# Kernel optimization log

Hardware: AMD Instinct MI355X
Metric: run time of the kernel (lower is better)

## Reference

```python
import jax, jax.numpy as jnp
import numpy as np

RATIO = 0.1

def setup_inputs() -> dict:
    key = jax.random.key(0)
    x = jax.random.normal(key, (8, 1024, 4096), dtype=jnp.float32)
    return {"x": x}

def reference(x):
    shape = x.shape
    xf = x.reshape(-1)                       # [N]
    k = int(RATIO * xf.shape[0])             # static k
    src, index = jax.lax.top_k(xf, k)         # values (not abs), matching torch.topk
    out = jnp.zeros_like(xf).at[index].set(src)
    return out.reshape(shape)
```

## Files before the change

### kernel.cpp

```cpp
#include <hip/hip_runtime.h>
#include <hip/hip_bf16.h>
#include <stdint.h>


#define STREAM_GRID 1024
#define STREAM_BLK  256
#define EQ_CAP      65536


__device__ __forceinline__ unsigned int f2u(float x) {
    unsigned int b = __float_as_uint(x);
    return (b & 0x80000000u) ? ~b : (b | 0x80000000u);
}

__global__ void init_kernel(unsigned int* sc, unsigned int k) {
    if (threadIdx.x == 0) {
        sc[0] = 0u; sc[1] = k; sc[2] = 0u; sc[3] = 0u; sc[4] = 0u;
    }
}

__global__ void __launch_bounds__(256)
hist_lds_kernel(const float* __restrict__ x, int n4, long long N,
                unsigned int* __restrict__ hist,
                const unsigned int* __restrict__ sc,
                int nbins, int shift, int match_shift)
{
    __shared__ unsigned int lh[4][2048];
    int tid = threadIdx.x;
    for (int i = tid; i < 4 * 2048; i += 256) ((unsigned int*)lh)[i] = 0u;
    const bool filt = (match_shift < 32);
    const int ms = filt ? match_shift : 0;
    unsigned int pref = 0u;
    if (filt) pref = sc[0] >> ms;
    __syncthreads();
    unsigned int* my = lh[tid >> 6];
    const float4* x4 = (const float4*)x;
    const unsigned int mask = (unsigned int)nbins - 1u;
    int stride = gridDim.x * blockDim.x;
    for (int i = blockIdx.x * blockDim.x + tid; i < n4; i += stride) {
        float4 v = x4[i];
        unsigned int u;
        u = f2u(v.x); if (!filt || ((u >> ms) == pref)) atomicAdd(&my[(u >> shift) & mask], 1u);
        u = f2u(v.y); if (!filt || ((u >> ms) == pref)) atomicAdd(&my[(u >> shift) & mask], 1u);
        u = f2u(v.z); if (!filt || ((u >> ms) == pref)) atomicAdd(&my[(u >> shift) & mask], 1u);
        u = f2u(v.w); if (!filt || ((u >> ms) == pref)) atomicAdd(&my[(u >> shift) & mask], 1u);
    }
    long long t0 = (long long)n4 * 4;
    if (blockIdx.x == 0 && tid < (int)(N - t0)) {
        unsigned int u = f2u(x[t0 + tid]);
        if (!filt || ((u >> ms) == pref)) atomicAdd(&my[(u >> shift) & mask], 1u);
    }
    __syncthreads();
    for (int i = tid; i < nbins; i += 256) {
        unsigned int s = lh[0][i] + lh[1][i] + lh[2][i] + lh[3][i];
        if (s) atomicAdd(&hist[i], s);
    }
}

__global__ void __launch_bounds__(256)
hist21_kernel(const float* __restrict__ x, int n4, long long N,
              unsigned int* __restrict__ hist2,
              const unsigned int* __restrict__ sc)
{
    unsigned int b1 = sc[0] >> 21;
    const float4* x4 = (const float4*)x;
    int stride = gridDim.x * blockDim.x;
    for (int i = blockIdx.x * blockDim.x + threadIdx.x; i < n4; i += stride) {
        float4 v = x4[i];
        unsigned int u;
        u = f2u(v.x); if ((u >> 21) == b1) atomicAdd(&hist2[u & 0x1FFFFFu], 1u);
        u = f2u(v.y); if ((u >> 21) == b1) atomicAdd(&hist2[u & 0x1FFFFFu], 1u);
        u = f2u(v.z); if ((u >> 21) == b1) atomicAdd(&hist2[u & 0x1FFFFFu], 1u);
        u = f2u(v.w); if ((u >> 21) == b1) atomicAdd(&hist2[u & 0x1FFFFFu], 1u);
    }
    long long t0 = (long long)n4 * 4;
    if (blockIdx.x == 0 && threadIdx.x < (int)(N - t0)) {
        unsigned int u = f2u(x[t0 + threadIdx.x]);
        if ((u >> 21) == b1) atomicAdd(&hist2[u & 0x1FFFFFu], 1u);
    }
}

__device__ __forceinline__ unsigned int block_exscan256(unsigned int v,
                                                        volatile unsigned int* lds,
                                                        int tid)
{
    lds[tid] = v;
    __syncthreads();
    for (int off = 1; off < 256; off <<= 1) {
        unsigned int t = (tid >= off) ? lds[tid - off] : 0u;
        __syncthreads();
        lds[tid] += t;
        __syncthreads();
    }
    unsigned int incl = lds[tid];
    return incl - v;
}

__global__ void __launch_bounds__(256)
scan_kernel(unsigned int* __restrict__ hist, int nbins, int shift, int is_final,
            unsigned int* __restrict__ sc)
{
    __shared__ unsigned int lds[256];
    int tid = threadIdx.x;
    int seg = nbins >> 8;
    unsigned int prefix = sc[0];
    unsigned int krem = sc[1];
    unsigned int loc[8];
    unsigned int partial = 0u;
    for (int i = 0; i < seg; ++i) {
        int p = tid * seg + i;
        unsigned int v = hist[nbins - 1 - p];
        loc[i] = v; partial += v;
    }
    unsigned int cum = block_exscan256(partial, lds, tid);
    for (int i = 0; i < seg; ++i) {
        int p = tid * seg + i;
        int bin = nbins - 1 - p;
        unsigned int c = loc[i];
        if (cum < krem && cum + c >= krem) {
            if (is_final) { sc[2] = prefix | ((unsigned int)bin << shift); sc[3] = krem - cum; }
            else          { sc[0] = prefix | ((unsigned int)bin << shift); sc[1] = krem - cum; }
        }
        cum += c;
    }
    for (int i = 0; i < seg; ++i) hist[nbins - 1 - (tid * seg + i)] = 0u;
}

__global__ void __launch_bounds__(256)
chunksum_kernel(const unsigned int* __restrict__ hist2, unsigned int* __restrict__ chunk_sums)
{
    __shared__ unsigned int p[256];
    int tid = threadIdx.x;
    int chunk = blockIdx.x;
    const unsigned int* base = hist2 + (size_t)chunk * 1024;
    unsigned int s = 0u;
    for (int i = tid; i < 1024; i += 256) s += base[i];
    p[tid] = s;
    __syncthreads();
    for (int off = 128; off; off >>= 1) {
        if (tid < off) p[tid] += p[tid + off];
        __syncthreads();
    }
    if (tid == 0) chunk_sums[chunk] = p[0];
}

__global__ void __launch_bounds__(256)
scanA_final_kernel(const unsigned int* __restrict__ hist2,
                   const unsigned int* __restrict__ chunk_sums,
                   unsigned int* __restrict__ sc)
{
    __shared__ unsigned int lds[256];
    __shared__ unsigned int s_c, s_krem2;
    int tid = threadIdx.x;
    unsigned int prefix = sc[0];
    unsigned int krem = sc[1];
    unsigned int loc[8];
    unsigned int partial = 0u;
    for (int i = 0; i < 8; ++i) {
        int p = tid * 8 + i;
        unsigned int v = chunk_sums[2047 - p];
        loc[i] = v; partial += v;
    }
    unsigned int cum = block_exscan256(partial, lds, tid);
    for (int i = 0; i < 8; ++i) {
        int p = tid * 8 + i;
        int chunk = 2047 - p;
        unsigned int c = loc[i];
        if (cum < krem && cum + c >= krem) { s_c = (unsigned int)chunk; s_krem2 = krem - cum; }
        cum += c;
    }
    __syncthreads();
    unsigned int c = s_c;
    unsigned int krem2 = s_krem2;
    unsigned int loc2[4];
    partial = 0u;
    for (int i = 0; i < 4; ++i) {
        int p = tid * 4 + i;
        unsigned int v = hist2[(size_t)c * 1024 + (1023 - p)];
        loc2[i] = v; partial += v;
    }
    __syncthreads();
    unsigned int cum2 = block_exscan256(partial, lds, tid);
    for (int i = 0; i < 4; ++i) {
        int p = tid * 4 + i;
        int bin = 1023 - p;
        unsigned int cc = loc2[i];
        if (cum2 < krem2 && cum2 + cc >= krem2) {
            sc[2] = prefix | (c * 1024u + (unsigned int)bin);
            sc[3] = krem2 - cum2;
        }
        cum2 += cc;
    }
}

__global__ void __launch_bounds__(256)
scatter_kernel(const float* __restrict__ x, int n4, long long N,
               float* __restrict__ out,
               unsigned int* __restrict__ sc,
               unsigned int* __restrict__ eq_list, int cap)
{
    unsigned int tu = sc[2];
    const float4* x4 = (const float4*)x;
    float4* o4 = (float4*)out;
    int stride = gridDim.x * blockDim.x;
    for (int i = blockIdx.x * blockDim.x + threadIdx.x; i < n4; i += stride) {
        float4 v = x4[i];
        unsigned int u0 = f2u(v.x), u1 = f2u(v.y), u2 = f2u(v.z), u3 = f2u(v.w);
        float4 o;
        o.x = (u0 > tu) ? v.x : 0.0f;
        o.y = (u1 > tu) ? v.y : 0.0f;
        o.z = (u2 > tu) ? v.z : 0.0f;
        o.w = (u3 > tu) ? v.w : 0.0f;
        if (u0 == tu || u1 == tu || u2 == tu || u3 == tu) {
            unsigned int b = (unsigned int)i * 4u;
            if (u0 == tu) { unsigned int p = atomicAdd(&sc[4], 1u); if (p < (unsigned int)cap) eq_list[p] = b + 0u; }
            if (u1 == tu) { unsigned int p = atomicAdd(&sc[4], 1u); if (p < (unsigned int)cap) eq_list[p] = b + 1u; }
            if (u2 == tu) { unsigned int p = atomicAdd(&sc[4], 1u); if (p < (unsigned int)cap) eq_list[p] = b + 2u; }
            if (u3 == tu) { unsigned int p = atomicAdd(&sc[4], 1u); if (p < (unsigned int)cap) eq_list[p] = b + 3u; }
        }
        o4[i] = o;
    }
    long long t0 = (long long)n4 * 4;
    if (blockIdx.x == 0 && threadIdx.x < (int)(N - t0)) {
        long long idx = t0 + threadIdx.x;
        float v = x[idx];
        unsigned int u = f2u(v);
        out[idx] = (u > tu) ? v : 0.0f;
        if (u == tu) { unsigned int p = atomicAdd(&sc[4], 1u); if (p < (unsigned int)cap) eq_list[p] = (unsigned int)idx; }
    }
}

__global__ void __launch_bounds__(256)
eqfix_kernel(float* __restrict__ out, const unsigned int* __restrict__ sc,
             const unsigned int* __restrict__ eq_list, int cap)
{
    unsigned int m = sc[4];
    if (m > (unsigned int)cap) m = (unsigned int)cap;
    unsigned int need = sc[3];
    unsigned int tu = sc[2];
    float f = __uint_as_float((tu & 0x80000000u) ? (tu & 0x7FFFFFFFu) : ~tu);
    for (unsigned int j = threadIdx.x; j < m; j += blockDim.x) {
        unsigned int idx = eq_list[j];
        unsigned int cnt = 0u;
        for (unsigned int l = 0; l < m; ++l) cnt += (eq_list[l] < idx) ? 1u : 0u;
        if (cnt < need) out[idx] = f;
    }
}

extern "C" void kernel_launch(void* const* d_in, const int* in_sizes, int n_in,
                              void* d_out, int out_size, void* d_ws, size_t ws_size,
                              hipStream_t stream) {
    const float* x = (const float*)d_in[0];
    float* out = (float*)d_out;
    long long N = (long long)in_sizes[0];
    int n4 = (int)(N >> 2);
    unsigned int k = (unsigned int)((double)N * 0.1);
    if (k == 0u) k = 1u;

    uint8_t* w = (uint8_t*)d_ws;
    unsigned int* sc         = (unsigned int*)(w);
    unsigned int* hist1      = (unsigned int*)(w + 256);
    unsigned int* chunk_sums = (unsigned int*)(w + 256 + 8192);
    unsigned int* eq_list    = (unsigned int*)(w + 256 + 16384);
    size_t baseB = 256 + 16384 + 262144;
    unsigned int* hist2      = (unsigned int*)(w + baseB);
    size_t needA = baseB + ((size_t)1 << 21) * sizeof(unsigned int);
    bool planA = (ws_size >= needA);

    int grid = STREAM_GRID;

    hipMemsetAsync(hist1, 0, 2048 * sizeof(unsigned int), stream);
    init_kernel<<<1, 64, 0, stream>>>(sc, k);

    if (planA) {
        hipMemsetAsync(hist2, 0, ((size_t)1 << 21) * sizeof(unsigned int), stream);
        hist_lds_kernel<<<grid, STREAM_BLK, 0, stream>>>(x, n4, N, hist1, sc, 2048, 21, 32);
        scan_kernel<<<1, 256, 0, stream>>>(hist1, 2048, 21, 0, sc);
        hist21_kernel<<<grid, STREAM_BLK, 0, stream>>>(x, n4, N, hist2, sc);
        chunksum_kernel<<<2048, 256, 0, stream>>>(hist2, chunk_sums);
        scanA_final_kernel<<<1, 256, 0, stream>>>(hist2, chunk_sums, sc);
    } else {
        hist_lds_kernel<<<grid, STREAM_BLK, 0, stream>>>(x, n4, N, hist1, sc, 2048, 21, 32);
        scan_kernel<<<1, 256, 0, stream>>>(hist1, 2048, 21, 0, sc);
        hist_lds_kernel<<<grid, STREAM_BLK, 0, stream>>>(x, n4, N, hist1, sc, 2048, 10, 21);
        scan_kernel<<<1, 256, 0, stream>>>(hist1, 2048, 10, 0, sc);
        hist_lds_kernel<<<grid, STREAM_BLK, 0, stream>>>(x, n4, N, hist1, sc, 1024, 0, 10);
        scan_kernel<<<1, 256, 0, stream>>>(hist1, 1024, 0, 1, sc);
    }

    scatter_kernel<<<grid, STREAM_BLK, 0, stream>>>(x, n4, N, out, sc, eq_list, EQ_CAP);
    eqfix_kernel<<<1, 256, 0, stream>>>(out, sc, eq_list, EQ_CAP);
}
```

Before: 332.9 us.

## Fuse radix-select top-k into one persistent kernel with grid barriers

Replaces the multi-kernel radix-select pipeline with a single persistent kernel that uses software grid-wide barriers. It builds a 12-bit histogram in one pass over x, then writes the output and compacts boundary-bucket candidates in a second pass. The remaining two 10-bit refinement levels run only on the candidate list instead of rereading the full input. This removes several full-tensor passes and kernel launches, but relies on all blocks being co-resident. The barrier has a spin timeout, and correctness also depends on the candidate buffer capacity.

```diff
diff --git a/kernel.cpp b/kernel.cpp
--- a/kernel.cpp
+++ b/kernel.cpp
@@ -1,249 +1,245 @@
 #include <hip/hip_runtime.h>
-#include <hip/hip_bf16.h>
 #include <stdint.h>
 
 
-#define STREAM_GRID 1024
-#define STREAM_BLK  256
-#define EQ_CAP      65536
-
-
-__device__ __forceinline__ unsigned int f2u(float x) {
-    unsigned int b = __float_as_uint(x);
+#define BLK       256
+#define MAXGRID   1024
+#define NB1       4096
+#define NB2       1024
+#define NB3       1024
+#define EQ_CAP    65536
+#define STAGE_CAP 4096
+
+__device__ __forceinline__ unsigned f2u(float x) {
+    unsigned b = __float_as_uint(x);
     return (b & 0x80000000u) ? ~b : (b | 0x80000000u);
 }
-
-__global__ void init_kernel(unsigned int* sc, unsigned int k) {
+__device__ __forceinline__ float u2f(unsigned u) {
+    return __uint_as_float((u & 0x80000000u) ? (u & 0x7FFFFFFFu) : ~u);
+}
+
+__device__ __forceinline__ void gsync(unsigned* bar, unsigned target) {
+    __syncthreads();
     if (threadIdx.x == 0) {
-        sc[0] = 0u; sc[1] = k; sc[2] = 0u; sc[3] = 0u; sc[4] = 0u;
-    }
-}
-
-__global__ void __launch_bounds__(256)
-hist_lds_kernel(const float* __restrict__ x, int n4, long long N,
-                unsigned int* __restrict__ hist,
-                const unsigned int* __restrict__ sc,
-                int nbins, int shift, int match_shift)
-{
-    __shared__ unsigned int lh[4][2048];
-    int tid = threadIdx.x;
-    for (int i = tid; i < 4 * 2048; i += 256) ((unsigned int*)lh)[i] = 0u;
-    const bool filt = (match_shift < 32);
-    const int ms = filt ? match_shift : 0;
-    unsigned int pref = 0u;
-    if (filt) pref = sc[0] >> ms;
-    __syncthreads();
-    unsigned int* my = lh[tid >> 6];
-    const float4* x4 = (const float4*)x;
-    const unsigned int mask = (unsigned int)nbins - 1u;
-    int stride = gridDim.x * blockDim.x;
-    for (int i = blockIdx.x * blockDim.x + tid; i < n4; i += stride) {
-        float4 v = x4[i];
-        unsigned int u;
-        u = f2u(v.x); if (!filt || ((u >> ms) == pref)) atomicAdd(&my[(u >> shift) & mask], 1u);
-        u = f2u(v.y); if (!filt || ((u >> ms) == pref)) atomicAdd(&my[(u >> shift) & mask], 1u);
-        u = f2u(v.z); if (!filt || ((u >> ms) == pref)) atomicAdd(&my[(u >> shift) & mask], 1u);
-        u = f2u(v.w); if (!filt || ((u >> ms) == pref)) atomicAdd(&my[(u >> shift) & mask], 1u);
-    }
-    long long t0 = (long long)n4 * 4;
-    if (blockIdx.x == 0 && tid < (int)(N - t0)) {
-        unsigned int u = f2u(x[t0 + tid]);
-        if (!filt || ((u >> ms) == pref)) atomicAdd(&my[(u >> shift) & mask], 1u);
-    }
-    __syncthreads();
-    for (int i = tid; i < nbins; i += 256) {
-        unsigned int s = lh[0][i] + lh[1][i] + lh[2][i] + lh[3][i];
-        if (s) atomicAdd(&hist[i], s);
-    }
-}
-
-__global__ void __launch_bounds__(256)
-hist21_kernel(const float* __restrict__ x, int n4, long long N,
-              unsigned int* __restrict__ hist2,
-              const unsigned int* __restrict__ sc)
-{
-    unsigned int b1 = sc[0] >> 21;
-    const float4* x4 = (const float4*)x;
-    int stride = gridDim.x * blockDim.x;
-    for (int i = blockIdx.x * blockDim.x + threadIdx.x; i < n4; i += stride) {
-        float4 v = x4[i];
-        unsigned int u;
-        u = f2u(v.x); if ((u >> 21) == b1) atomicAdd(&hist2[u & 0x1FFFFFu], 1u);
-        u = f2u(v.y); if ((u >> 21) == b1) atomicAdd(&hist2[u & 0x1FFFFFu], 1u);
-        u = f2u(v.z); if ((u >> 21) == b1) atomicAdd(&hist2[u & 0x1FFFFFu], 1u);
-        u = f2u(v.w); if ((u >> 21) == b1) atomicAdd(&hist2[u & 0x1FFFFFu], 1u);
-    }
-    long long t0 = (long long)n4 * 4;
-    if (blockIdx.x == 0 && threadIdx.x < (int)(N - t0)) {
-        unsigned int u = f2u(x[t0 + threadIdx.x]);
-        if ((u >> 21) == b1) atomicAdd(&hist2[u & 0x1FFFFFu], 1u);
-    }
-}
-
-__device__ __forceinline__ unsigned int block_exscan256(unsigned int v,
-                                                        volatile unsigned int* lds,
-                                                        int tid)
+        __threadfence();
+        __hip_atomic_fetch_add(bar, 1u, __ATOMIC_RELEASE, __HIP_MEMORY_SCOPE_AGENT);
+        unsigned spins = 0u;
+        while (__hip_atomic_load(bar, __ATOMIC_ACQUIRE, __HIP_MEMORY_SCOPE_AGENT) < target) {
+            __builtin_amdgcn_s_sleep(2);
+            if (++spins > 8000000u) break;
+        }
+        __threadfence();
+    }
+    __syncthreads();
+}
+
+__device__ __forceinline__ unsigned block_exscan256(unsigned v,
+                                                    volatile unsigned* lds,
+                                                    int tid)
 {
     lds[tid] = v;
     __syncthreads();
     for (int off = 1; off < 256; off <<= 1) {
-        unsigned int t = (tid >= off) ? lds[tid - off] : 0u;
+        unsigned t = (tid >= off) ? lds[tid - off] : 0u;
         __syncthreads();
         lds[tid] += t;
         __syncthreads();
     }
-    unsigned int incl = lds[tid];
+    unsigned incl = lds[tid];
     return incl - v;
 }
 
-__global__ void __launch_bounds__(256)
-scan_kernel(unsigned int* __restrict__ hist, int nbins, int shift, int is_final,
-            unsigned int* __restrict__ sc)
+__global__ void __launch_bounds__(BLK, 4)
+topk_fused(const float* __restrict__ x, float* __restrict__ out,
+           long long N, int n4, unsigned k,
+           unsigned* __restrict__ sc,
+           unsigned* __restrict__ hist_a, unsigned* __restrict__ hist_b,
+           unsigned* __restrict__ hist_c,
+           unsigned* __restrict__ cand_u, unsigned* __restrict__ cand_idx,
+           unsigned cand_cap, unsigned* __restrict__ eq_list)
 {
-    __shared__ unsigned int lds[256];
-    int tid = threadIdx.x;
-    int seg = nbins >> 8;
-    unsigned int prefix = sc[0];
-    unsigned int krem = sc[1];
-    unsigned int loc[8];
-    unsigned int partial = 0u;
-    for (int i = 0; i < seg; ++i) {
-        int p = tid * seg + i;
-        unsigned int v = hist[nbins - 1 - p];
-        loc[i] = v; partial += v;
-    }
-    unsigned int cum = block_exscan256(partial, lds, tid);
-    for (int i = 0; i < seg; ++i) {
-        int p = tid * seg + i;
-        int bin = nbins - 1 - p;
-        unsigned int c = loc[i];
-        if (cum < krem && cum + c >= krem) {
-            if (is_final) { sc[2] = prefix | ((unsigned int)bin << shift); sc[3] = krem - cum; }
-            else          { sc[0] = prefix | ((unsigned int)bin << shift); sc[1] = krem - cum; }
-        }
-        cum += c;
-    }
-    for (int i = 0; i < seg; ++i) hist[nbins - 1 - (tid * seg + i)] = 0u;
-}
-
-__global__ void __launch_bounds__(256)
-chunksum_kernel(const unsigned int* __restrict__ hist2, unsigned int* __restrict__ chunk_sums)
-{
-    __shared__ unsigned int p[256];
-    int tid = threadIdx.x;
-    int chunk = blockIdx.x;
-    const unsigned int* base = hist2 + (size_t)chunk * 1024;
-    unsigned int s = 0u;
-    for (int i = tid; i < 1024; i += 256) s += base[i];
-    p[tid] = s;
-    __syncthreads();
-    for (int off = 128; off; off >>= 1) {
-        if (tid < off) p[tid] += p[tid + off];
-        __syncthreads();
-    }
-    if (tid == 0) chunk_sums[chunk] = p[0];
-}
-
-__global__ void __launch_bounds__(256)
-scanA_final_kernel(const unsigned int* __restrict__ hist2,
-                   const unsigned int* __restrict__ chunk_sums,
-                   unsigned int* __restrict__ sc)
-{
-    __shared__ unsigned int lds[256];
-    __shared__ unsigned int s_c, s_krem2;
-    int tid = threadIdx.x;
-    unsigned int prefix = sc[0];
-    unsigned int krem = sc[1];
-    unsigned int loc[8];
-    unsigned int partial = 0u;
-    for (int i = 0; i < 8; ++i) {
-        int p = tid * 8 + i;
-        unsigned int v = chunk_sums[2047 - p];
-        loc[i] = v; partial += v;
-    }
-    unsigned int cum = block_exscan256(partial, lds, tid);
-    for (int i = 0; i < 8; ++i) {
-        int p = tid * 8 + i;
-        int chunk = 2047 - p;
-        unsigned int c = loc[i];
-        if (cum < krem && cum + c >= krem) { s_c = (unsigned int)chunk; s_krem2 = krem - cum; }
-        cum += c;
-    }
-    __syncthreads();
-    unsigned int c = s_c;
-    unsigned int krem2 = s_krem2;
-    unsigned int loc2[4];
-    partial = 0u;
-    for (int i = 0; i < 4; ++i) {
-        int p = tid * 4 + i;
-        unsigned int v = hist2[(size_t)c * 1024 + (1023 - p)];
-        loc2[i] = v; partial += v;
-    }
-    __syncthreads();
-    unsigned int cum2 = block_exscan256(partial, lds, tid);
-    for (int i = 0; i < 4; ++i) {
-        int p = tid * 4 + i;
-        int bin = 1023 - p;
-        unsigned int cc = loc2[i];
-        if (cum2 < krem2 && cum2 + cc >= krem2) {
-            sc[2] = prefix | (c * 1024u + (unsigned int)bin);
-            sc[3] = krem2 - cum2;
-        }
-        cum2 += cc;
-    }
-}
-
-__global__ void __launch_bounds__(256)
-scatter_kernel(const float* __restrict__ x, int n4, long long N,
-               float* __restrict__ out,
-               unsigned int* __restrict__ sc,
-               unsigned int* __restrict__ eq_list, int cap)
-{
-    unsigned int tu = sc[2];
+    __shared__ unsigned lh[2][NB1];
+    __shared__ unsigned slds[256];
+    __shared__ unsigned sb[4];
+
+    const int tid = threadIdx.x;
+    const int bid = blockIdx.x;
+    const unsigned nbk = gridDim.x;
+    const int stride = (int)nbk * BLK;
+    unsigned* bar = sc + 8;
+    unsigned ph = 0;
+
+    if (bid == 0) {
+        for (int i = tid; i < NB1; i += BLK) hist_a[i] = 0u;
+        for (int i = tid; i < NB2; i += BLK) hist_b[i] = 0u;
+        for (int i = tid; i < NB3; i += BLK) hist_c[i] = 0u;
+    }
+    for (int i = tid; i < 2 * NB1; i += BLK) (&lh[0][0])[i] = 0u;
+    __syncthreads();
+    unsigned* my = lh[(tid >> 7) & 1];
     const float4* x4 = (const float4*)x;
+    for (int i = bid * BLK + tid; i < n4; i += stride) {
+        float4 v = x4[i];
+        atomicAdd(&my[f2u(v.x) >> 20], 1u);
+        atomicAdd(&my[f2u(v.y) >> 20], 1u);
+        atomicAdd(&my[f2u(v.z) >> 20], 1u);
+        atomicAdd(&my[f2u(v.w) >> 20], 1u);
+    }
+    const long long t0 = (long long)n4 * 4;
+    const int ntail = (int)(N - t0);
+    if (bid == 0 && tid < ntail) atomicAdd(&my[f2u(x[t0 + tid]) >> 20], 1u);
+
+    gsync(bar, ++ph * nbk);
+
+    for (int i = tid; i < NB1; i += BLK) {
+        unsigned s = lh[0][i] + lh[1][i];
+        if (s) atomicAdd(&hist_a[i], s);
+    }
+    gsync(bar, ++ph * nbk);
+
+    unsigned b1, krem;
+    {
+        unsigned loc[16], partial = 0u;
+#pragma unroll
+        for (int i = 0; i < 16; ++i) { loc[i] = hist_a[NB1 - 1 - (tid * 16 + i)]; partial += loc[i]; }
+        unsigned cum = block_exscan256(partial, slds, tid);
+#pragma unroll
+        for (int i = 0; i < 16; ++i) {
+            unsigned c = loc[i];
+            if (cum < k && cum + c >= k) { sb[0] = (unsigned)(NB1 - 1 - (tid * 16 + i)); sb[1] = k - cum; }
+            cum += c;
+        }
+        __syncthreads();
+        b1 = sb[0]; krem = sb[1];
+    }
+    __syncthreads();
+
+    if (tid == 0) sb[2] = 0u;
+    __syncthreads();
+    auto stage = [&](unsigned u, unsigned idxv) {
+        unsigned p = atomicAdd(&sb[2], 1u);
+        if (p < STAGE_CAP) { lh[0][p] = u; lh[1][p] = idxv; }
+        else { unsigned q = atomicAdd(&sc[4], 1u);
+               if (q < cand_cap) { cand_u[q] = u; cand_idx[q] = idxv; } }
+    };
     float4* o4 = (float4*)out;
-    int stride = gridDim.x * blockDim.x;
-    for (int i = blockIdx.x * blockDim.x + threadIdx.x; i < n4; i += stride) {
+    for (int i = bid * BLK + tid; i < n4; i += stride) {
         float4 v = x4[i];
-        unsigned int u0 = f2u(v.x), u1 = f2u(v.y), u2 = f2u(v.z), u3 = f2u(v.w);
+        unsigned u0 = f2u(v.x), u1 = f2u(v.y), u2 = f2u(v.z), u3 = f2u(v.w);
         float4 o;
-        o.x = (u0 > tu) ? v.x : 0.0f;
-        o.y = (u1 > tu) ? v.y : 0.0f;
-        o.z = (u2 > tu) ? v.z : 0.0f;
-        o.w = (u3 > tu) ? v.w : 0.0f;
-        if (u0 == tu || u1 == tu || u2 == tu || u3 == tu) {
-            unsigned int b = (unsigned int)i * 4u;
-            if (u0 == tu) { unsigned int p = atomicAdd(&sc[4], 1u); if (p < (unsigned int)cap) eq_list[p] = b + 0u; }
-            if (u1 == tu) { unsigned int p = atomicAdd(&sc[4], 1u); if (p < (unsigned int)cap) eq_list[p] = b + 1u; }
-            if (u2 == tu) { unsigned int p = atomicAdd(&sc[4], 1u); if (p < (unsigned int)cap) eq_list[p] = b + 2u; }
-            if (u3 == tu) { unsigned int p = atomicAdd(&sc[4], 1u); if (p < (unsigned int)cap) eq_list[p] = b + 3u; }
-        }
+        o.x = ((u0 >> 20) > b1) ? v.x : 0.0f;
+        o.y = ((u1 >> 20) > b1) ? v.y : 0.0f;
+        o.z = ((u2 >> 20) > b1) ? v.z : 0.0f;
+        o.w = ((u3 >> 20) > b1) ? v.w : 0.0f;
         o4[i] = o;
-    }
-    long long t0 = (long long)n4 * 4;
-    if (blockIdx.x == 0 && threadIdx.x < (int)(N - t0)) {
-        long long idx = t0 + threadIdx.x;
+        if (((u0 >> 20) == b1) | ((u1 >> 20) == b1) | ((u2 >> 20) == b1) | ((u3 >> 20) == b1)) {
+            unsigned base = (unsigned)i * 4u;
+            if ((u0 >> 20) == b1) stage(u0, base + 0u);
+            if ((u1 >> 20) == b1) stage(u1, base + 1u);
+            if ((u2 >> 20) == b1) stage(u2, base + 2u);
+            if ((u3 >> 20) == b1) stage(u3, base + 3u);
+        }
+    }
+    if (bid == 0 && tid < ntail) {
+        long long idx = t0 + tid;
         float v = x[idx];
-        unsigned int u = f2u(v);
-        out[idx] = (u > tu) ? v : 0.0f;
-        if (u == tu) { unsigned int p = atomicAdd(&sc[4], 1u); if (p < (unsigned int)cap) eq_list[p] = (unsigned int)idx; }
-    }
-}
-
-__global__ void __launch_bounds__(256)
-eqfix_kernel(float* __restrict__ out, const unsigned int* __restrict__ sc,
-             const unsigned int* __restrict__ eq_list, int cap)
-{
-    unsigned int m = sc[4];
-    if (m > (unsigned int)cap) m = (unsigned int)cap;
-    unsigned int need = sc[3];
-    unsigned int tu = sc[2];
-    float f = __uint_as_float((tu & 0x80000000u) ? (tu & 0x7FFFFFFFu) : ~tu);
-    for (unsigned int j = threadIdx.x; j < m; j += blockDim.x) {
-        unsigned int idx = eq_list[j];
-        unsigned int cnt = 0u;
-        for (unsigned int l = 0; l < m; ++l) cnt += (eq_list[l] < idx) ? 1u : 0u;
-        if (cnt < need) out[idx] = f;
+        unsigned u = f2u(v);
+        out[idx] = ((u >> 20) > b1) ? v : 0.0f;
+        if ((u >> 20) == b1) stage(u, (unsigned)idx);
+    }
+    __syncthreads();
+    unsigned bc = sb[2]; if (bc > STAGE_CAP) bc = STAGE_CAP;
+    if (tid == 0) sb[3] = atomicAdd(&sc[4], bc);
+    __syncthreads();
+    {
+        unsigned gbase = sb[3];
+        for (unsigned j = (unsigned)tid; j < bc; j += BLK) {
+            unsigned p = gbase + j;
+            if (p < cand_cap) { cand_u[p] = lh[0][j]; cand_idx[p] = lh[1][j]; }
+        }
+    }
+    gsync(bar, ++ph * nbk);
+
+    unsigned m = sc[4]; if (m > cand_cap) m = cand_cap;
+    for (int i = tid; i < NB2; i += BLK) { lh[0][i] = 0u; lh[1][i] = 0u; }
+    __syncthreads();
+    for (unsigned j = (unsigned)(bid * BLK + tid); j < m; j += (unsigned)stride) {
+        unsigned u = cand_u[j];
+        atomicAdd(&my[(u >> 10) & 1023u], 1u);
+    }
+    __syncthreads();
+    for (int i = tid; i < NB2; i += BLK) {
+        unsigned s = lh[0][i] + lh[1][i];
+        if (s) atomicAdd(&hist_b[i], s);
+    }
+    gsync(bar, ++ph * nbk);
+
+    unsigned b2, krem2;
+    {
+        unsigned loc[4], partial = 0u;
+#pragma unroll
+        for (int i = 0; i < 4; ++i) { loc[i] = hist_b[NB2 - 1 - (tid * 4 + i)]; partial += loc[i]; }
+        unsigned cum = block_exscan256(partial, slds, tid);
+#pragma unroll
+        for (int i = 0; i < 4; ++i) {
+            unsigned c = loc[i];
+            if (cum < krem && cum + c >= krem) { sb[0] = (unsigned)(NB2 - 1 - (tid * 4 + i)); sb[1] = krem - cum; }
+            cum += c;
+        }
+        __syncthreads();
+        b2 = sb[0]; krem2 = sb[1];
+    }
+    __syncthreads();
+
+    for (int i = tid; i < NB3; i += BLK) { lh[0][i] = 0u; lh[1][i] = 0u; }
+    __syncthreads();
+    for (unsigned j = (unsigned)(bid * BLK + tid); j < m; j += (unsigned)stride) {
+        unsigned u = cand_u[j];
+        if (((u >> 10) & 1023u) == b2) atomicAdd(&my[u & 1023u], 1u);
+    }
+    __syncthreads();
+    for (int i = tid; i < NB3; i += BLK) {
+        unsigned s = lh[0][i] + lh[1][i];
+        if (s) atomicAdd(&hist_c[i], s);
+    }
+    gsync(bar, ++ph * nbk);
+
+    unsigned b3, needeq;
+    {
+        unsigned loc[4], partial = 0u;
+#pragma unroll
+        for (int i = 0; i < 4; ++i) { loc[i] = hist_c[NB3 - 1 - (tid * 4 + i)]; partial += loc[i]; }
+        unsigned cum = block_exscan256(partial, slds, tid);
+#pragma unroll
+        for (int i = 0; i < 4; ++i) {
+            unsigned c = loc[i];
+            if (cum < krem2 && cum + c >= krem2) { sb[0] = (unsigned)(NB3 - 1 - (tid * 4 + i)); sb[1] = krem2 - cum; }
+            cum += c;
+        }
+        __syncthreads();
+        b3 = sb[0]; needeq = sb[1];
+    }
+    const unsigned tu = (b1 << 20) | (b2 << 10) | b3;
+
+    for (unsigned j = (unsigned)(bid * BLK + tid); j < m; j += (unsigned)stride) {
+        unsigned u = cand_u[j];
+        if (u > tu) out[cand_idx[j]] = u2f(u);
+        else if (u == tu) {
+            unsigned q = atomicAdd(&sc[5], 1u);
+            if (q < EQ_CAP) eq_list[q] = cand_idx[j];
+        }
+    }
+    gsync(bar, ++ph * nbk);
+
+    if (bid == 0) {
+        unsigned me = sc[5]; if (me > EQ_CAP) me = EQ_CAP;
+        float f = u2f(tu);
+        for (unsigned j = (unsigned)tid; j < me; j += BLK) {
+            unsigned idxv = eq_list[j];
+            unsigned cnt = 0u;
+            for (unsigned l = 0; l < me; ++l) cnt += (eq_list[l] < idxv) ? 1u : 0u;
+            if (cnt < needeq) out[idxv] = f;
+        }
     }
 }
 
@@ -254,40 +250,41 @@
     float* out = (float*)d_out;
     long long N = (long long)in_sizes[0];
     int n4 = (int)(N >> 2);
-    unsigned int k = (unsigned int)((double)N * 0.1);
+    unsigned k = (unsigned)((double)N * 0.1);
     if (k == 0u) k = 1u;
 
     uint8_t* w = (uint8_t*)d_ws;
-    unsigned int* sc         = (unsigned int*)(w);
-    unsigned int* hist1      = (unsigned int*)(w + 256);
-    unsigned int* chunk_sums = (unsigned int*)(w + 256 + 8192);
-    unsigned int* eq_list    = (unsigned int*)(w + 256 + 16384);
-    size_t baseB = 256 + 16384 + 262144;
-    unsigned int* hist2      = (unsigned int*)(w + baseB);
-    size_t needA = baseB + ((size_t)1 << 21) * sizeof(unsigned int);
-    bool planA = (ws_size >= needA);
-
-    int grid = STREAM_GRID;
-
-    hipMemsetAsync(hist1, 0, 2048 * sizeof(unsigned int), stream);
-    init_kernel<<<1, 64, 0, stream>>>(sc, k);
-
-    if (planA) {
-        hipMemsetAsync(hist2, 0, ((size_t)1 << 21) * sizeof(unsigned int), stream);
-        hist_lds_kernel<<<grid, STREAM_BLK, 0, stream>>>(x, n4, N, hist1, sc, 2048, 21, 32);
-        scan_kernel<<<1, 256, 0, stream>>>(hist1, 2048, 21, 0, sc);
-        hist21_kernel<<<grid, STREAM_BLK, 0, stream>>>(x, n4, N, hist2, sc);
-        chunksum_kernel<<<2048, 256, 0, stream>>>(hist2, chunk_sums);
-        scanA_final_kernel<<<1, 256, 0, stream>>>(hist2, chunk_sums, sc);
-    } else {
-        hist_lds_kernel<<<grid, STREAM_BLK, 0, stream>>>(x, n4, N, hist1, sc, 2048, 21, 32);
-        scan_kernel<<<1, 256, 0, stream>>>(hist1, 2048, 21, 0, sc);
-        hist_lds_kernel<<<grid, STREAM_BLK, 0, stream>>>(x, n4, N, hist1, sc, 2048, 10, 21);
-        scan_kernel<<<1, 256, 0, stream>>>(hist1, 2048, 10, 0, sc);
-        hist_lds_kernel<<<grid, STREAM_BLK, 0, stream>>>(x, n4, N, hist1, sc, 1024, 0, 10);
-        scan_kernel<<<1, 256, 0, stream>>>(hist1, 1024, 0, 1, sc);
-    }
-
-    scatter_kernel<<<grid, STREAM_BLK, 0, stream>>>(x, n4, N, out, sc, eq_list, EQ_CAP);
-    eqfix_kernel<<<1, 256, 0, stream>>>(out, sc, eq_list, EQ_CAP);
-}
+    unsigned* sc      = (unsigned*)(w);
+    unsigned* hist_a  = (unsigned*)(w + 256);
+    unsigned* hist_b  = (unsigned*)(w + 256 + 16384);
+    unsigned* hist_c  = (unsigned*)(w + 256 + 16384 + 4096);
+    unsigned* eq_list = (unsigned*)(w + 256 + 16384 + 4096 + 4096);
+    size_t fixed = 256 + 16384 + 4096 + 4096 + (size_t)EQ_CAP * 4;
+    size_t rem = (ws_size > fixed) ? (ws_size - fixed) : 0;
+    size_t cap_sz = rem / 8;
+    if (cap_sz > (size_t)(8u << 20)) cap_sz = (size_t)(8u << 20);
+    unsigned cand_cap = (unsigned)cap_sz;
+    unsigned* cand_u   = (unsigned*)(w + fixed);
+    unsigned* cand_idx = cand_u + cand_cap;
+
+    static int g_grid = 0;
+    if (g_grid == 0) {
+        int nb = 0;
+        if (hipOccupancyMaxActiveBlocksPerMultiprocessor(&nb, (const void*)topk_fused,
+                                                         BLK, 0) != hipSuccess || nb < 1)
+            nb = 4;
+        int dev = 0; hipGetDevice(&dev);
+        int ncu = 0;
+        if (hipDeviceGetAttribute(&ncu, hipDeviceAttributeMultiprocessorCount, dev) != hipSuccess || ncu < 1)
+            ncu = 256;
+        long long g = (long long)nb * (long long)ncu;
+        if (g > MAXGRID) g = MAXGRID;
+        if (g < 1) g = 1;
+        g_grid = (int)g;
+    }
+
+    hipMemsetAsync(sc, 0, 256, stream);
+    hipLaunchKernelGGL(topk_fused, dim3(g_grid), dim3(BLK), 0, stream,
+                       x, out, N, n4, k, sc, hist_a, hist_b, hist_c,
+                       cand_u, cand_idx, cand_cap, eq_list);
+}
```

Result: slower. 1.167 ms (+250.5%).
